# Kernel tuning notes

Hardware: AMD Instinct MI355X
Metric: run time of the kernel (lower is better)

## Reference

```python
import jax, jax.numpy as jnp
import numpy as np

K_SELECTED = 8  # config.num_selected_heads


def setup_inputs() -> dict:
    key = jax.random.key(0)
    k1, k2 = jax.random.split(key, 2)
    B, N, H, L = 4, 4096, 2048, 64
    x = jax.random.normal(k1, (B, N, H), dtype=jnp.float32)
    W_r = jax.random.normal(k2, (L, H), dtype=jnp.float32) * 0.02  # nn.Linear weight (L, H), no bias
    expert_bias = jnp.zeros((L,), dtype=jnp.float32)
    active_mask = jnp.ones((B, N), dtype=bool)
    return {"x": x, "W_r": W_r, "expert_bias": expert_bias, "active_mask": active_mask}


def reference(x, W_r, expert_bias, active_mask):
    L = expert_bias.shape[0]
    K = K_SELECTED
    # logits = x @ W_r.T  (bias-free routing projection)
    logits = jnp.einsum('bnh,lh->bnl', x, W_r)
    routing_scores = jax.nn.softmax(logits, axis=-1)            # unbiased probs
    biased_scores = jax.nn.softmax(logits + expert_bias, -1)    # biased probs for selection
    # top-K on biased scores -> selected head indices (B, N, K)
    _, selected_heads = jax.lax.top_k(biased_scores, K)
    # gather unbiased scores at selected indices and renormalize
    gathered = jnp.take_along_axis(routing_scores, selected_heads, axis=-1)
    routing_probs = gathered / gathered.sum(axis=-1, keepdims=True)
    # scatter into assignment mask: one-hot over L summed over K slots
    assignment_mask = jax.nn.one_hot(selected_heads, L, dtype=x.dtype).sum(axis=-2)  # (B, N, L)
    am = active_mask.astype(x.dtype)
    active_assignments = assignment_mask * am[..., None]
    num_active_assignments = am.sum() * K
    routing_freqs = active_assignments.sum(axis=(0, 1)) / num_active_assignments  # (L,)
    # LoadBalanceLoss.apply(expert_bias, routing_freqs): squared-imbalance value
    inv_L = 1.0 / L
    load_balance_loss = L * jnp.sum((routing_freqs - inv_L) ** 2)
    max_vio = jax.lax.stop_gradient(L * jnp.max(routing_freqs - inv_L))
    return selected_heads, routing_probs, load_balance_loss, max_vio
```

## Files before the change

kernel.cpp:

```cpp
#include <hip/hip_runtime.h>
#include <stdint.h>
#include <math.h>

constexpr int H     = 2048;
constexpr int L     = 64;
constexpr int K_SEL = 8;

constexpr int TMR   = 64;
constexpr int KS    = 8;
constexpr int KSLAB = H / KS;
constexpr int BK    = 32;
constexpr int SX    = 68;
constexpr int SW    = 68;

constexpr float EPS_GAP = 1e-4f;

constexpr int WS_COUNTS = 0;
constexpr int WS_NFIX   = 128;
constexpr int WS_LIST   = 256;
constexpr int WS_WT     = 16640;
constexpr int WS_LOGITS = 147712;

__global__ __launch_bounds__(256)
void prep(const float* __restrict__ Wr, float* __restrict__ Wt,
          unsigned int* __restrict__ wsu, float* __restrict__ logits)
{
    const int t = threadIdx.x, b = blockIdx.x;
    if (b == 32) {
        if (t < L + 1) wsu[WS_COUNTS + t] = 0u;
        if (t == 0)    wsu[WS_NFIX] = 0u;
        return;
    }
    if (b >= 33) {
        float4* p = (float4*)logits;
        const int zb = b - 33;
        #pragma unroll
        for (int q = 0; q < 16; ++q)
            p[(size_t)zb * 4096 + q * 256 + t] = make_float4(0.f, 0.f, 0.f, 0.f);
        return;
    }
    __shared__ float tile[64 * 65];
    const int k0 = b * 64;
    {
        const int l = t >> 2, kq = (t & 3) * 16;
        #pragma unroll
        for (int j = 0; j < 4; ++j) {
            float4 v = *(const float4*)(Wr + (size_t)l * H + k0 + kq + 4 * j);
            int k = kq + 4 * j;
            tile[(k + 0) * 65 + l] = v.x;
            tile[(k + 1) * 65 + l] = v.y;
            tile[(k + 2) * 65 + l] = v.z;
            tile[(k + 3) * 65 + l] = v.w;
        }
    }
    __syncthreads();
    {
        const int k = t >> 2, lq = (t & 3) * 16;
        #pragma unroll
        for (int j = 0; j < 4; ++j) {
            int l2 = lq + 4 * j;
            float4 o = make_float4(tile[k * 65 + l2], tile[k * 65 + l2 + 1],
                                   tile[k * 65 + l2 + 2], tile[k * 65 + l2 + 3]);
            *(float4*)(Wt + (size_t)(k0 + k) * L + l2) = o;
        }
    }
}

__global__ __launch_bounds__(64, 2)
void router_gemm(const float* __restrict__ x, const float* __restrict__ Wr,
                 float* __restrict__ logits)
{
    __shared__ __align__(16) float smem[2 * BK * SX];
    float* xs  = smem;
    float* wls = smem + BK * SX;

    const int t  = threadIdx.x;
    const int rb = blockIdx.x & 255;
    const int ks = blockIdx.x >> 8;
    const int R0 = rb * TMR;
    const int k0 = ks * KSLAB;

    const int r0 = 8 * (t >> 3);
    const int c0 = 8 * (t & 7);
    const int u  = t >> 2;
    const int a  = t & 3;

    float acc[8][8] = {};
    float4 xg[8], wg[8];

    const float* xp = x  + (size_t)(R0 + u) * H + k0 + 4 * a;
    const float* wp = Wr + (size_t)u * H        + k0 + 4 * a;

    #pragma unroll
    for (int j = 0; j < 4; ++j)
        #pragma unroll
        for (int m = 0; m < 2; ++m) {
            xg[2 * j + m] = *(const float4*)(xp + (size_t)(16 * j) * H + 16 * m);
            wg[2 * j + m] = *(const float4*)(wp + (size_t)(16 * j) * H + 16 * m);
        }

    for (int s = 0; s < KSLAB / BK; ++s) {
        #pragma unroll
        for (int j = 0; j < 4; ++j)
            #pragma unroll
            for (int m = 0; m < 2; ++m) {
                const float4 vx = xg[2 * j + m], vw = wg[2 * j + m];
                const int k = 4 * a + 16 * m, rc = u + 16 * j;
                xs [(k + 0) * SX + rc] = vx.x;
                xs [(k + 1) * SX + rc] = vx.y;
                xs [(k + 2) * SX + rc] = vx.z;
                xs [(k + 3) * SX + rc] = vx.w;
                wls[(k + 0) * SW + rc] = vw.x;
                wls[(k + 1) * SW + rc] = vw.y;
                wls[(k + 2) * SW + rc] = vw.z;
                wls[(k + 3) * SW + rc] = vw.w;
            }
        __syncthreads();

        if (s + 1 < KSLAB / BK) {
            const int kb = BK * (s + 1);
            #pragma unroll
            for (int j = 0; j < 4; ++j)
                #pragma unroll
                for (int m = 0; m < 2; ++m) {
                    xg[2 * j + m] = *(const float4*)(xp + (size_t)(16 * j) * H + kb + 16 * m);
                    wg[2 * j + m] = *(const float4*)(wp + (size_t)(16 * j) * H + kb + 16 * m);
                }
        }

        #pragma unroll 8
        for (int kk = 0; kk < BK; ++kk) {
            const float4 xv0 = *(const float4*)(xs  + kk * SX + r0);
            const float4 xv1 = *(const float4*)(xs  + kk * SX + r0 + 4);
            const float4 wv0 = *(const float4*)(wls + kk * SW + c0);
            const float4 wv1 = *(const float4*)(wls + kk * SW + c0 + 4);
            const float xr[8] = {xv0.x, xv0.y, xv0.z, xv0.w, xv1.x, xv1.y, xv1.z, xv1.w};
            const float wc[8] = {wv0.x, wv0.y, wv0.z, wv0.w, wv1.x, wv1.y, wv1.z, wv1.w};
            #pragma unroll
            for (int i = 0; i < 8; ++i)
                #pragma unroll
                for (int j = 0; j < 8; ++j)
                    acc[i][j] = fmaf(xr[i], wc[j], acc[i][j]);
        }
        __syncthreads();
    }

    float* lg = smem;
    #pragma unroll
    for (int i = 0; i < 8; ++i)
        #pragma unroll
        for (int j = 0; j < 8; ++j)
            lg[(r0 + i) * 65 + c0 + j] = acc[i][j];
    __syncthreads();

    float* dst = logits + (size_t)R0 * L + t;
    #pragma unroll 8
    for (int i = 0; i < TMR; ++i)
        atomicAdd(dst + (size_t)i * L, lg[i * 65 + t]);
}

constexpr int TE = 64;
__global__ __launch_bounds__(64)
void router_topk(const float* __restrict__ logits, const float* __restrict__ bias,
                 const unsigned char* __restrict__ am,
                 float* __restrict__ out_sel, float* __restrict__ out_probs,
                 unsigned int* __restrict__ g_counts, unsigned int* __restrict__ nfix,
                 unsigned int* __restrict__ list)
{
    __shared__ float lg[TE][L + 1];
    __shared__ float bs[L];
    __shared__ unsigned int cnt[L + 1];

    const int t  = threadIdx.x;
    const int R0 = blockIdx.x * TE;

    bs[t]  = bias[t];
    cnt[t] = 0;
    if (t == 0) cnt[L] = 0;

    const float4* src = (const float4*)(logits + (size_t)R0 * L);
    #pragma unroll
    for (int q = 0; q < 16; ++q) {
        const int idx = t + 64 * q;
        const float4 v = src[idx];
        const int row = idx >> 4;
        const int c   = (idx & 15) * 4;
        lg[row][c + 0] = v.x;
        lg[row][c + 1] = v.y;
        lg[row][c + 2] = v.z;
        lg[row][c + 3] = v.w;
    }
    __syncthreads();

    {
        const int grow = R0 + t;
        unsigned long long chosen = 0ull;
        int idx[K_SEL];
        float prev = 0.f, gmin = INFINITY;
        for (int kk = 0; kk < K_SEL + 1; ++kk) {
            float best = -INFINITY; int bi = 0;
            for (int l = 0; l < L; ++l) {
                if ((chosen >> l) & 1ull) continue;
                float v = lg[t][l] + bs[l];
                if (v > best) { best = v; bi = l; }
            }
            if (kk > 0) gmin = fminf(gmin, prev - best);
            prev = best;
            if (kk < K_SEL) { chosen |= 1ull << bi; idx[kk] = bi; }
        }

        if (gmin < EPS_GAP) {
            unsigned int p = atomicAdd(nfix, 1u);
            list[p] = (unsigned int)grow;
        } else {
            float zv[K_SEL], mx = -INFINITY;
            #pragma unroll
            for (int kk = 0; kk < K_SEL; ++kk) { zv[kk] = lg[t][idx[kk]]; mx = fmaxf(mx, zv[kk]); }
            float e[K_SEL], ssum = 0.f;
            #pragma unroll
            for (int kk = 0; kk < K_SEL; ++kk) { e[kk] = expf(zv[kk] - mx); ssum += e[kk]; }
            #pragma unroll
            for (int kk = 0; kk < K_SEL; ++kk) {
                out_sel[(size_t)grow * K_SEL + kk]   = (float)idx[kk];
                out_probs[(size_t)grow * K_SEL + kk] = e[kk] / ssum;
            }
            if (am[grow]) {
                atomicAdd(&cnt[L], 1u);
                #pragma unroll
                for (int kk = 0; kk < K_SEL; ++kk) atomicAdd(&cnt[idx[kk]], 1u);
            }
        }
    }
    __syncthreads();
    if (cnt[t]) atomicAdd(&g_counts[t], cnt[t]);
    if (t == 0 && cnt[L]) atomicAdd(&g_counts[L], cnt[L]);
}

__global__ __launch_bounds__(256)
void fixup(const float* __restrict__ x, const float* __restrict__ Wt,
           const float* __restrict__ bias, const unsigned char* __restrict__ am,
           const unsigned int* __restrict__ nfix, const unsigned int* __restrict__ list,
           float* __restrict__ out_sel, float* __restrict__ out_probs,
           unsigned int* __restrict__ g_counts)
{
    const int lane = threadIdx.x & 63;
    const int wid  = (blockIdx.x << 2) | (threadIdx.x >> 6);
    const int nw   = gridDim.x << 2;
    const int n    = (int)*nfix;
    const double bl = (double)bias[lane];

    for (int i = wid; i < n; i += nw) {
        const int row = (int)list[i];
        const float* xr = x + (size_t)row * H;
        double a0 = 0.0, a1 = 0.0, a2 = 0.0, a3 = 0.0;
        #pragma unroll 2
        for (int k = 0; k < H; k += 16) {
            float4 x0 = *(const float4*)(xr + k);
            float4 x1 = *(const float4*)(xr + k + 4);
            float4 x2 = *(const float4*)(xr + k + 8);
            float4 x3 = *(const float4*)(xr + k + 12);
            a0 = fma((double)x0.x, (double)Wt[(k +  0) * L + lane], a0);
            a1 = fma((double)x0.y, (double)Wt[(k +  1) * L + lane], a1);
            a2 = fma((double)x0.z, (double)Wt[(k +  2) * L + lane], a2);
            a3 = fma((double)x0.w, (double)Wt[(k +  3) * L + lane], a3);
            a0 = fma((double)x1.x, (double)Wt[(k +  4) * L + lane], a0);
            a1 = fma((double)x1.y, (double)Wt[(k +  5) * L + lane], a1);
            a2 = fma((double)x1.z, (double)Wt[(k +  6) * L + lane], a2);
            a3 = fma((double)x1.w, (double)Wt[(k +  7) * L + lane], a3);
            a0 = fma((double)x2.x, (double)Wt[(k +  8) * L + lane], a0);
            a1 = fma((double)x2.y, (double)Wt[(k +  9) * L + lane], a1);
            a2 = fma((double)x2.z, (double)Wt[(k + 10) * L + lane], a2);
            a3 = fma((double)x2.w, (double)Wt[(k + 11) * L + lane], a3);
            a0 = fma((double)x3.x, (double)Wt[(k + 12) * L + lane], a0);
            a1 = fma((double)x3.y, (double)Wt[(k + 13) * L + lane], a1);
            a2 = fma((double)x3.z, (double)Wt[(k + 14) * L + lane], a2);
            a3 = fma((double)x3.w, (double)Wt[(k + 15) * L + lane], a3);
        }
        double acc = (a0 + a1) + (a2 + a3);

        double v = acc + bl;
        int    widx[K_SEL];
        double wlog[K_SEL];
        #pragma unroll
        for (int kk = 0; kk < K_SEL; ++kk) {
            double mv = v; int mi = lane;
            #pragma unroll
            for (int off = 32; off; off >>= 1) {
                double ov = __shfl_xor(mv, off);
                int    oi = __shfl_xor(mi, off);
                if (ov > mv || (ov == mv && oi < mi)) { mv = ov; mi = oi; }
            }
            widx[kk] = mi;
            wlog[kk] = __shfl(acc, mi);
            if (lane == mi) v = -INFINITY;
        }

        double mx = -INFINITY;
        #pragma unroll
        for (int kk = 0; kk < K_SEL; ++kk) mx = fmax(mx, wlog[kk]);
        float e[K_SEL], ssum = 0.f;
        #pragma unroll
        for (int kk = 0; kk < K_SEL; ++kk) { e[kk] = expf((float)(wlog[kk] - mx)); ssum += e[kk]; }

        if (lane < K_SEL) {
            out_sel[(size_t)row * K_SEL + lane]   = (float)widx[lane];
            out_probs[(size_t)row * K_SEL + lane] = e[lane] / ssum;
        }
        if (am[row]) {
            if (lane < K_SEL)  atomicAdd(&g_counts[widx[lane]], 1u);
            if (lane == K_SEL) atomicAdd(&g_counts[L], 1u);
        }
    }
}

__global__ void router_finalize(const unsigned int* __restrict__ g_counts,
                                float* __restrict__ out_scalars)
{
    const int l = threadIdx.x;
    const float denom = (float)g_counts[L] * (float)K_SEL;
    const float f = (float)g_counts[l] / denom;
    float d  = f - 1.0f / (float)L;
    float sq = d * d;
    #pragma unroll
    for (int o = 32; o > 0; o >>= 1) {
        sq += __shfl_down(sq, o);
        d = fmaxf(d, __shfl_down(d, o));
    }
    if (l == 0) {
        out_scalars[0] = (float)L * sq;
        out_scalars[1] = (float)L * d;
    }
}

extern "C" void kernel_launch(void* const* d_in, const int* in_sizes, int n_in,
                              void* d_out, int out_size, void* d_ws, size_t ws_size,
                              hipStream_t stream)
{
    const float* x          = (const float*)d_in[0];
    const float* Wr         = (const float*)d_in[1];
    const float* bias       = (const float*)d_in[2];
    const unsigned char* am = (const unsigned char*)d_in[3];
    float* out = (float*)d_out;
    float* wsf = (float*)d_ws;
    unsigned int* wsu = (unsigned int*)d_ws;

    const int rows = in_sizes[3];

    float* out_sel   = out;
    float* out_probs = out + (size_t)rows * K_SEL;
    float* out_scal  = out + (size_t)rows * K_SEL * 2;

    hipLaunchKernelGGL(prep,            dim3(97),              dim3(256), 0, stream,
                       Wr, wsf + WS_WT, wsu, wsf + WS_LOGITS);
    hipLaunchKernelGGL(router_gemm,     dim3((rows / TMR) * KS), dim3(64), 0, stream,
                       x, Wr, wsf + WS_LOGITS);
    hipLaunchKernelGGL(router_topk,     dim3(rows / TE),       dim3(64),  0, stream,
                       wsf + WS_LOGITS, bias, am, out_sel, out_probs,
                       wsu + WS_COUNTS, wsu + WS_NFIX, wsu + WS_LIST);
    hipLaunchKernelGGL(fixup,           dim3(256),             dim3(256), 0, stream,
                       x, wsf + WS_WT, bias, am, wsu + WS_NFIX, wsu + WS_LIST,
                       out_sel, out_probs, wsu + WS_COUNTS);
    hipLaunchKernelGGL(router_finalize, dim3(1),               dim3(64),  0, stream,
                       wsu + WS_COUNTS, out_scal);
}
```

Baseline: 319.4 us.

## Enlarge GEMM row tile to 256 with 256 threads and parallelise top-k per row

The router GEMM block grows from 64 threads covering 64 rows to 256 threads covering 256 rows. Each thread loads one contiguous x row segment, and the W tile staged in shared memory is reused across four times more rows. Split-K partial logits are flushed through shared memory in four 64-row chunks with atomics. The top-k kernel now gives each row to 8 lanes, which do a register-resident argmax with xor shuffles instead of one thread scanning 64 values serially. This adds more shared memory and register pressure per block and produces fewer GEMM blocks (512).

```diff
diff --git a/kernel.cpp b/kernel.cpp
--- a/kernel.cpp
+++ b/kernel.cpp
@@ -6,12 +6,12 @@
 constexpr int L     = 64;
 constexpr int K_SEL = 8;
 
-constexpr int TMR   = 64;
+constexpr int TMR   = 256;
 constexpr int KS    = 8;
 constexpr int KSLAB = H / KS;
 constexpr int BK    = 32;
-constexpr int SX    = 68;
-constexpr int SW    = 68;
+constexpr int SXR   = 260;
+constexpr int SWR   = 68;
 
 constexpr float EPS_GAP = 1e-4f;
 
@@ -66,174 +66,186 @@
     }
 }
 
-__global__ __launch_bounds__(64, 2)
+__global__ __launch_bounds__(256, 2)
 void router_gemm(const float* __restrict__ x, const float* __restrict__ Wr,
                  float* __restrict__ logits)
 {
-    __shared__ __align__(16) float smem[2 * BK * SX];
-    float* xs  = smem;
-    float* wls = smem + BK * SX;
-
-    const int t  = threadIdx.x;
-    const int rb = blockIdx.x & 255;
-    const int ks = blockIdx.x >> 8;
-    const int R0 = rb * TMR;
-    const int k0 = ks * KSLAB;
-
-    const int r0 = 8 * (t >> 3);
-    const int c0 = 8 * (t & 7);
-    const int u  = t >> 2;
-    const int a  = t & 3;
+    __shared__ __align__(16) float xs[BK * SXR];
+    __shared__ __align__(16) float ws[BK * SWR];
+    __shared__ __align__(16) float lg[64 * 65];
+
+    const int t   = threadIdx.x;
+    const int rb  = blockIdx.x & 63;
+    const int ks  = blockIdx.x >> 6;
+    const int R0  = rb * TMR;
+    const int k0  = ks * KSLAB;
+    const int g   = t >> 3;
+    const int j   = t & 7;
+    const int r0  = 8 * g, c0 = 8 * j;
+    const int wid = t >> 6;
+    const int lane = t & 63;
 
     float acc[8][8] = {};
-    float4 xg[8], wg[8];
-
-    const float* xp = x  + (size_t)(R0 + u) * H + k0 + 4 * a;
-    const float* wp = Wr + (size_t)u * H        + k0 + 4 * a;
+    float4 xg[8], wg[2];
+
+    const float* xp = x  + (size_t)(R0 + t) * H + k0;
+    const float* wp = Wr + (size_t)lane * H     + k0 + 8 * wid;
 
     #pragma unroll
-    for (int j = 0; j < 4; ++j)
-        #pragma unroll
-        for (int m = 0; m < 2; ++m) {
-            xg[2 * j + m] = *(const float4*)(xp + (size_t)(16 * j) * H + 16 * m);
-            wg[2 * j + m] = *(const float4*)(wp + (size_t)(16 * j) * H + 16 * m);
-        }
+    for (int q = 0; q < 8; ++q) xg[q] = *(const float4*)(xp + 4 * q);
+    wg[0] = *(const float4*)(wp);
+    wg[1] = *(const float4*)(wp + 4);
 
     for (int s = 0; s < KSLAB / BK; ++s) {
         #pragma unroll
-        for (int j = 0; j < 4; ++j)
-            #pragma unroll
-            for (int m = 0; m < 2; ++m) {
-                const float4 vx = xg[2 * j + m], vw = wg[2 * j + m];
-                const int k = 4 * a + 16 * m, rc = u + 16 * j;
-                xs [(k + 0) * SX + rc] = vx.x;
-                xs [(k + 1) * SX + rc] = vx.y;
-                xs [(k + 2) * SX + rc] = vx.z;
-                xs [(k + 3) * SX + rc] = vx.w;
-                wls[(k + 0) * SW + rc] = vw.x;
-                wls[(k + 1) * SW + rc] = vw.y;
-                wls[(k + 2) * SW + rc] = vw.z;
-                wls[(k + 3) * SW + rc] = vw.w;
-            }
+        for (int q = 0; q < 8; ++q) {
+            const float4 v = xg[q];
+            xs[(4 * q + 0) * SXR + t] = v.x;
+            xs[(4 * q + 1) * SXR + t] = v.y;
+            xs[(4 * q + 2) * SXR + t] = v.z;
+            xs[(4 * q + 3) * SXR + t] = v.w;
+        }
+        #pragma unroll
+        for (int e = 0; e < 2; ++e) {
+            const float4 v = wg[e];
+            const int kw = 8 * wid + 4 * e;
+            ws[(kw + 0) * SWR + lane] = v.x;
+            ws[(kw + 1) * SWR + lane] = v.y;
+            ws[(kw + 2) * SWR + lane] = v.z;
+            ws[(kw + 3) * SWR + lane] = v.w;
+        }
         __syncthreads();
 
         if (s + 1 < KSLAB / BK) {
             const int kb = BK * (s + 1);
             #pragma unroll
-            for (int j = 0; j < 4; ++j)
-                #pragma unroll
-                for (int m = 0; m < 2; ++m) {
-                    xg[2 * j + m] = *(const float4*)(xp + (size_t)(16 * j) * H + kb + 16 * m);
-                    wg[2 * j + m] = *(const float4*)(wp + (size_t)(16 * j) * H + kb + 16 * m);
-                }
+            for (int q = 0; q < 8; ++q) xg[q] = *(const float4*)(xp + kb + 4 * q);
+            wg[0] = *(const float4*)(wp + kb);
+            wg[1] = *(const float4*)(wp + kb + 4);
         }
 
         #pragma unroll 8
         for (int kk = 0; kk < BK; ++kk) {
-            const float4 xv0 = *(const float4*)(xs  + kk * SX + r0);
-            const float4 xv1 = *(const float4*)(xs  + kk * SX + r0 + 4);
-            const float4 wv0 = *(const float4*)(wls + kk * SW + c0);
-            const float4 wv1 = *(const float4*)(wls + kk * SW + c0 + 4);
+            const float4 xv0 = *(const float4*)(xs + kk * SXR + r0);
+            const float4 xv1 = *(const float4*)(xs + kk * SXR + r0 + 4);
+            const float4 wv0 = *(const float4*)(ws + kk * SWR + c0);
+            const float4 wv1 = *(const float4*)(ws + kk * SWR + c0 + 4);
             const float xr[8] = {xv0.x, xv0.y, xv0.z, xv0.w, xv1.x, xv1.y, xv1.z, xv1.w};
             const float wc[8] = {wv0.x, wv0.y, wv0.z, wv0.w, wv1.x, wv1.y, wv1.z, wv1.w};
             #pragma unroll
             for (int i = 0; i < 8; ++i)
                 #pragma unroll
-                for (int j = 0; j < 8; ++j)
-                    acc[i][j] = fmaf(xr[i], wc[j], acc[i][j]);
+                for (int jj = 0; jj < 8; ++jj)
+                    acc[i][jj] = fmaf(xr[i], wc[jj], acc[i][jj]);
         }
         __syncthreads();
     }
 
-    float* lg = smem;
-    #pragma unroll
-    for (int i = 0; i < 8; ++i)
-        #pragma unroll
-        for (int j = 0; j < 8; ++j)
-            lg[(r0 + i) * 65 + c0 + j] = acc[i][j];
-    __syncthreads();
-
-    float* dst = logits + (size_t)R0 * L + t;
-    #pragma unroll 8
-    for (int i = 0; i < TMR; ++i)
-        atomicAdd(dst + (size_t)i * L, lg[i * 65 + t]);
-}
-
-constexpr int TE = 64;
-__global__ __launch_bounds__(64)
+    for (int c = 0; c < 4; ++c) {
+        if (wid == c) {
+            const int lr = 8 * (g & 7);
+            #pragma unroll
+            for (int i = 0; i < 8; ++i)
+                #pragma unroll
+                for (int jj = 0; jj < 8; ++jj)
+                    lg[(lr + i) * 65 + c0 + jj] = acc[i][jj];
+        }
+        __syncthreads();
+        float* dst = logits + (size_t)(R0 + 64 * c) * L;
+        #pragma unroll
+        for (int p = 0; p < 16; ++p) {
+            const int idx = t + 256 * p;
+            const int row = idx >> 6, col = idx & 63;
+            atomicAdd(dst + (size_t)row * L + col, lg[row * 65 + col]);
+        }
+        __syncthreads();
+    }
+}
+
+constexpr int TKR = 32;
+__global__ __launch_bounds__(256)
 void router_topk(const float* __restrict__ logits, const float* __restrict__ bias,
                  const unsigned char* __restrict__ am,
                  float* __restrict__ out_sel, float* __restrict__ out_probs,
                  unsigned int* __restrict__ g_counts, unsigned int* __restrict__ nfix,
                  unsigned int* __restrict__ list)
 {
-    __shared__ float lg[TE][L + 1];
     __shared__ float bs[L];
     __shared__ unsigned int cnt[L + 1];
 
-    const int t  = threadIdx.x;
-    const int R0 = blockIdx.x * TE;
-
-    bs[t]  = bias[t];
-    cnt[t] = 0;
-    if (t == 0) cnt[L] = 0;
-
-    const float4* src = (const float4*)(logits + (size_t)R0 * L);
+    const int t   = threadIdx.x;
+    const int j   = t & 7;
+    const int row = blockIdx.x * TKR + (t >> 3);
+
+    if (t < L)     bs[t]  = bias[t];
+    if (t < L + 1) cnt[t] = 0;
+    __syncthreads();
+
+    float rv[8], lv[8];
+    {
+        const float* lp = logits + (size_t)row * L + 8 * j;
+        const float4 v0 = *(const float4*)(lp);
+        const float4 v1 = *(const float4*)(lp + 4);
+        rv[0] = v0.x; rv[1] = v0.y; rv[2] = v0.z; rv[3] = v0.w;
+        rv[4] = v1.x; rv[5] = v1.y; rv[6] = v1.z; rv[7] = v1.w;
+        #pragma unroll
+        for (int i = 0; i < 8; ++i) lv[i] = rv[i] + bs[8 * j + i];
+    }
+
+    unsigned msk = 0;
+    int   selidx[K_SEL];
+    float selraw[K_SEL];
+    float prev = 0.f, gmin = INFINITY;
+
     #pragma unroll
-    for (int q = 0; q < 16; ++q) {
-        const int idx = t + 64 * q;
-        const float4 v = src[idx];
-        const int row = idx >> 4;
-        const int c   = (idx & 15) * 4;
-        lg[row][c + 0] = v.x;
-        lg[row][c + 1] = v.y;
-        lg[row][c + 2] = v.z;
-        lg[row][c + 3] = v.w;
+    for (int kk = 0; kk < K_SEL + 1; ++kk) {
+        float best = -INFINITY; int bi = 1 << 30; float braw = 0.f;
+        #pragma unroll
+        for (int i = 0; i < 8; ++i) {
+            const bool free_ = !((msk >> i) & 1u);
+            if (free_ && lv[i] > best) { best = lv[i]; bi = 8 * j + i; braw = rv[i]; }
+        }
+        #pragma unroll
+        for (int off = 1; off <= 4; off <<= 1) {
+            const float ov  = __shfl_xor(best, off);
+            const int   oi  = __shfl_xor(bi,   off);
+            const float orw = __shfl_xor(braw, off);
+            if (ov > best || (ov == best && oi < bi)) { best = ov; bi = oi; braw = orw; }
+        }
+        if (kk > 0) gmin = fminf(gmin, prev - best);
+        prev = best;
+        if (kk < K_SEL) {
+            if ((bi >> 3) == j) msk |= 1u << (bi & 7);
+            selidx[kk] = bi;
+            selraw[kk] = braw;
+        }
+    }
+
+    if (gmin < EPS_GAP) {
+        if (j == 0) {
+            unsigned int p = atomicAdd(nfix, 1u);
+            list[p] = (unsigned int)row;
+        }
+    } else {
+        float mx = -INFINITY;
+        #pragma unroll
+        for (int kk = 0; kk < K_SEL; ++kk) mx = fmaxf(mx, selraw[kk]);
+        float e[K_SEL], ssum = 0.f;
+        #pragma unroll
+        for (int kk = 0; kk < K_SEL; ++kk) { e[kk] = expf(selraw[kk] - mx); ssum += e[kk]; }
+        float myp = 0.f; int myi = 0;
+        #pragma unroll
+        for (int kk = 0; kk < K_SEL; ++kk)
+            if (kk == j) { myp = e[kk] / ssum; myi = selidx[kk]; }
+        out_sel  [(size_t)row * K_SEL + j] = (float)myi;
+        out_probs[(size_t)row * K_SEL + j] = myp;
+        if (am[row]) {
+            atomicAdd(&cnt[myi], 1u);
+            if (j == 0) atomicAdd(&cnt[L], 1u);
+        }
     }
     __syncthreads();
-
-    {
-        const int grow = R0 + t;
-        unsigned long long chosen = 0ull;
-        int idx[K_SEL];
-        float prev = 0.f, gmin = INFINITY;
-        for (int kk = 0; kk < K_SEL + 1; ++kk) {
-            float best = -INFINITY; int bi = 0;
-            for (int l = 0; l < L; ++l) {
-                if ((chosen >> l) & 1ull) continue;
-                float v = lg[t][l] + bs[l];
-                if (v > best) { best = v; bi = l; }
-            }
-            if (kk > 0) gmin = fminf(gmin, prev - best);
-            prev = best;
-            if (kk < K_SEL) { chosen |= 1ull << bi; idx[kk] = bi; }
-        }
-
-        if (gmin < EPS_GAP) {
-            unsigned int p = atomicAdd(nfix, 1u);
-            list[p] = (unsigned int)grow;
-        } else {
-            float zv[K_SEL], mx = -INFINITY;
-            #pragma unroll
-            for (int kk = 0; kk < K_SEL; ++kk) { zv[kk] = lg[t][idx[kk]]; mx = fmaxf(mx, zv[kk]); }
-            float e[K_SEL], ssum = 0.f;
-            #pragma unroll
-            for (int kk = 0; kk < K_SEL; ++kk) { e[kk] = expf(zv[kk] - mx); ssum += e[kk]; }
-            #pragma unroll
-            for (int kk = 0; kk < K_SEL; ++kk) {
-                out_sel[(size_t)grow * K_SEL + kk]   = (float)idx[kk];
-                out_probs[(size_t)grow * K_SEL + kk] = e[kk] / ssum;
-            }
-            if (am[grow]) {
-                atomicAdd(&cnt[L], 1u);
-                #pragma unroll
-                for (int kk = 0; kk < K_SEL; ++kk) atomicAdd(&cnt[idx[kk]], 1u);
-            }
-        }
-    }
-    __syncthreads();
-    if (cnt[t]) atomicAdd(&g_counts[t], cnt[t]);
-    if (t == 0 && cnt[L]) atomicAdd(&g_counts[L], cnt[L]);
+    if (t < L + 1 && cnt[t]) atomicAdd(&g_counts[t], cnt[t]);
 }
 
 __global__ __launch_bounds__(256)
@@ -350,16 +362,16 @@
     float* out_probs = out + (size_t)rows * K_SEL;
     float* out_scal  = out + (size_t)rows * K_SEL * 2;
 
-    hipLaunchKernelGGL(prep,            dim3(97),              dim3(256), 0, stream,
+    hipLaunchKernelGGL(prep,            dim3(97),                dim3(256), 0, stream,
                        Wr, wsf + WS_WT, wsu, wsf + WS_LOGITS);
-    hipLaunchKernelGGL(router_gemm,     dim3((rows / TMR) * KS), dim3(64), 0, stream,
+    hipLaunchKernelGGL(router_gemm,     dim3((rows / TMR) * KS), dim3(256), 0, stream,
                        x, Wr, wsf + WS_LOGITS);
-    hipLaunchKernelGGL(router_topk,     dim3(rows / TE),       dim3(64),  0, stream,
+    hipLaunchKernelGGL(router_topk,     dim3(rows / TKR),        dim3(256), 0, stream,
                        wsf + WS_LOGITS, bias, am, out_sel, out_probs,
                        wsu + WS_COUNTS, wsu + WS_NFIX, wsu + WS_LIST);
-    hipLaunchKernelGGL(fixup,           dim3(256),             dim3(256), 0, stream,
+    hipLaunchKernelGGL(fixup,           dim3(256),               dim3(256), 0, stream,
                        x, wsf + WS_WT, bias, am, wsu + WS_NFIX, wsu + WS_LIST,
                        out_sel, out_probs, wsu + WS_COUNTS);
-    hipLaunchKernelGGL(router_finalize, dim3(1),               dim3(64),  0, stream,
+    hipLaunchKernelGGL(router_finalize, dim3(1),                 dim3(64),  0, stream,
                        wsu + WS_COUNTS, out_scal);
 }
```

New measurement: 296.9 us. -7.1%, faster.
